# Performance work log

Measured on AMD Instinct MI355X. Metric: run time of the kernel, lower is better.

Reference implementation:

```python
import jax, jax.numpy as jnp
import numpy as np

D_MODEL = 1024
N_HEADS = 16
DIM_HEAD = D_MODEL // N_HEADS
SCALE = DIM_HEAD ** (-0.5)
B, T = 8, 1024


def setup_inputs() -> dict:
    key = jax.random.key(0)
    k1, k2, k3 = jax.random.split(key, 3)
    x = jax.random.normal(k1, (B, T, D_MODEL), dtype=jnp.float32)
    m = jnp.ones((B, T), dtype=jnp.float32)  # padding mask (1 = keep)
    w_qkv = jax.random.normal(k2, (3 * D_MODEL, D_MODEL), dtype=jnp.float32) * (D_MODEL ** -0.5)
    w_out = jax.random.normal(k3, (D_MODEL, D_MODEL), dtype=jnp.float32) * (D_MODEL ** -0.5)
    b_out = jnp.zeros((D_MODEL,), dtype=jnp.float32)
    return {"x": x, "m": m, "w_qkv": w_qkv, "w_out": w_out, "b_out": b_out, "l": T}


def reference(x, m, w_qkv, w_out, b_out, l):
    b, t, dm = x.shape
    qkv = jnp.einsum('btd,ed->bte', x, w_qkv)  # (b,t,3*d_model)
    q, k, v = jnp.split(qkv, 3, axis=-1)
    rs = lambda a: a.reshape(b, t, N_HEADS, DIM_HEAD)
    q, k, v = rs(q), rs(k), rs(v)
    e = jnp.einsum('bihd,bjhd->bijh', q, k) * SCALE  # (b,i,j,h)
    # combined padding + causal mask
    kpm = m[:, :, None] * m[:, None, :]              # (b,i,j)
    kpm = jnp.tril(kpm)[..., None]                   # (b,i,j,1)
    neg = -jnp.finfo(e.dtype).max
    e = jnp.where(kpm == 0, neg, e)
    a = jax.nn.softmax(e, axis=2)                    # softmax over j
    o = jnp.einsum('bijh,bjhd->bihd', a, v).reshape(b, t, dm)
    o = jnp.einsum('btd,ed->bte', o, w_out) + b_out
    # dropout is identity in eval mode
    return o * m[..., None]
```

## Files before the change

### kernel.cpp

```cpp
#include <hip/hip_runtime.h>
#include <cstdint>
#include <cstddef>

typedef unsigned short u16;
typedef __bf16 bf16;
typedef bf16 __attribute__((ext_vector_type(4))) bf16x4;
typedef bf16 __attribute__((ext_vector_type(8))) bf16x8;
typedef float __attribute__((ext_vector_type(4))) f32x4;
typedef u16 __attribute__((ext_vector_type(8))) u16x8;

#define QSCALE 0.18033688011112042f

__device__ __forceinline__ u16 f2b(float x) {
  unsigned u = __float_as_uint(x);
  unsigned r = (u + 0x7fffu + ((u >> 16) & 1u)) >> 16;
  return (u16)r;
}

__device__ __forceinline__ void gl_lds16(const void* g, void* lds) {
  __builtin_amdgcn_global_load_lds(
      (const __attribute__((address_space(1))) unsigned int*)g,
      (__attribute__((address_space(3))) unsigned int*)lds, 16, 0, 0);
}

__device__ __forceinline__ bf16x8 frag(const u16* base, int row, int kchunk) {
  const int c = kchunk ^ (row & 7);
  return *(const bf16x8*)(base + row * 64 + c * 8);
}
__device__ __forceinline__ void stage_tile4(const u16* gbase, int K, char* lbase,
                                            int wave, int lane) {
#pragma unroll
  for (int i = 0; i < 4; ++i) {
    const int q = wave * 64 + lane + i * 256;
    const int r = q >> 3, c = (q & 7) ^ (r & 7);
    gl_lds16(gbase + (size_t)r * K + c * 8, lbase + i * 4096 + wave * 1024);
  }
}

__device__ __forceinline__ bf16x8 frag32(const u16* base, int row, int kchunk) {
  const int c = kchunk ^ ((row >> 1) & 3);
  return *(const bf16x8*)(base + row * 32 + c * 8);
}
__device__ __forceinline__ void stage32(const u16* gbase, int K, char* lbase,
                                        int wave, int lane) {
  const int q0 = wave * 64 + lane;
  const int r0 = q0 >> 2, c0 = (q0 & 3) ^ ((r0 >> 1) & 3);
  gl_lds16(gbase + (size_t)r0 * K + c0 * 8, lbase + wave * 1024);
  const int q1 = q0 + 256;
  const int r1 = q1 >> 2, c1 = (q1 & 3) ^ ((r1 >> 1) & 3);
  gl_lds16(gbase + (size_t)r1 * K + c1 * 8, lbase + 4096 + wave * 1024);
}

__global__ __launch_bounds__(256) void castk(const float* __restrict__ in,
                                             u16* __restrict__ out, int n) {
  int i = (blockIdx.x * 256 + threadIdx.x) * 8;
  if (i >= n) return;
  float4 a = *(const float4*)(in + i);
  float4 b = *(const float4*)(in + i + 4);
  u16x8 v;
  v[0] = f2b(a.x); v[1] = f2b(a.y); v[2] = f2b(a.z); v[3] = f2b(a.w);
  v[4] = f2b(b.x); v[5] = f2b(b.y); v[6] = f2b(b.z); v[7] = f2b(b.w);
  *(u16x8*)(out + i) = v;
}

__global__ __launch_bounds__(256, 4) void gemm_qkv(
    const u16* __restrict__ A, const u16* __restrict__ B,
    u16* __restrict__ Qo, u16* __restrict__ Ko, u16* __restrict__ Vo) {
  __shared__ u16 As[2][128 * 32];
  __shared__ u16 Bs[2][128 * 32];
  const int tid = threadIdx.x;
  const int lane = tid & 63, wave = tid >> 6;
  const int fr = lane & 15, fg = lane >> 4;
  const int wr = wave >> 1, wc = wave & 1;
  const int bid = blockIdx.x;
  const int bm = bid & 63, bn = bid >> 6;
  const int K = 1024;
  const u16* Ab = A + (size_t)bm * 128 * K;
  const u16* Bb = B + (size_t)bn * 128 * K;

  f32x4 acc[4][4] = {};

  stage32(Ab, K, (char*)&As[0][0], wave, lane);
  stage32(Bb, K, (char*)&Bs[0][0], wave, lane);
  __syncthreads();

  int cur = 0;
#pragma unroll 1
  for (int t = 0; t < 32; ++t) {
    if (t < 31) {
      stage32(Ab + (size_t)(t + 1) * 32, K, (char*)&As[cur ^ 1][0], wave, lane);
      stage32(Bb + (size_t)(t + 1) * 32, K, (char*)&Bs[cur ^ 1][0], wave, lane);
    }
    bf16x8 af[4], bfv[4];
#pragma unroll
    for (int mi = 0; mi < 4; ++mi)
      af[mi] = frag32(&As[cur][0], wr * 64 + mi * 16 + fr, fg);
#pragma unroll
    for (int ni = 0; ni < 4; ++ni)
      bfv[ni] = frag32(&Bs[cur][0], wc * 64 + ni * 16 + fr, fg);
#pragma unroll
    for (int mi = 0; mi < 4; ++mi)
#pragma unroll
      for (int ni = 0; ni < 4; ++ni)
        acc[mi][ni] = __builtin_amdgcn_mfma_f32_16x16x32_bf16(
            af[mi], bfv[ni], acc[mi][ni], 0, 0, 0);
    __syncthreads();
    cur ^= 1;
  }

  const int gr0 = bm * 128 + wr * 64;
  const int gc0 = bn * 128 + wc * 64;
#pragma unroll
  for (int mi = 0; mi < 4; ++mi) {
    const int rb = gr0 + mi * 16 + fg * 4;
    const int b = rb >> 10, t = rb & 1023;
#pragma unroll
    for (int ni = 0; ni < 4; ++ni) {
      const int c = gc0 + ni * 16 + fr;
      const int region = c >> 10, cc = c & 1023;
      const int h = cc >> 6, d = cc & 63;
      const size_t bh = (size_t)(b * 16 + h);
      if (region == 0) {
#pragma unroll
        for (int g = 0; g < 4; ++g)
          Qo[(bh * 1024 + t + g) * 64 + d] = f2b(acc[mi][ni][g] * QSCALE);
      } else if (region == 1) {
#pragma unroll
        for (int g = 0; g < 4; ++g)
          Ko[(bh * 1024 + t + g) * 64 + d] = f2b(acc[mi][ni][g]);
      } else {
        ushort4 pv;
        pv.x = f2b(acc[mi][ni][0]);
        pv.y = f2b(acc[mi][ni][1]);
        pv.z = f2b(acc[mi][ni][2]);
        pv.w = f2b(acc[mi][ni][3]);
        *(ushort4*)(Vo + (bh * 64 + d) * 1024 + t) = pv;
      }
    }
  }
}

__global__ __launch_bounds__(256) void gemm_bt2(
    const u16* __restrict__ A, const u16* __restrict__ B,
    float* __restrict__ Co, const float* __restrict__ bias,
    const float* __restrict__ msk) {
  __shared__ u16 As[2][128 * 64];
  __shared__ u16 Bs[2][128 * 64];
  const int tid = threadIdx.x;
  const int lane = tid & 63, wave = tid >> 6;
  const int fr = lane & 15, fg = lane >> 4;
  const int wr = wave >> 1, wc = wave & 1;
  const int bid = blockIdx.x;
  const int bm = bid & 63, bn = bid >> 6;
  const int K = 1024, N = 1024;
  const u16* Ab = A + (size_t)bm * 128 * K;
  const u16* Bb = B + (size_t)bn * 128 * K;

  f32x4 acc[4][4] = {};

  stage_tile4(Ab, K, (char*)&As[0][0], wave, lane);
  stage_tile4(Bb, K, (char*)&Bs[0][0], wave, lane);
  __syncthreads();

  int cur = 0;
#pragma unroll 1
  for (int t = 0; t < 16; ++t) {
    if (t < 15) {
      stage_tile4(Ab + (size_t)(t + 1) * 64, K, (char*)&As[cur ^ 1][0], wave, lane);
      stage_tile4(Bb + (size_t)(t + 1) * 64, K, (char*)&Bs[cur ^ 1][0], wave, lane);
    }
    bf16x8 af[4][2], bfv[4][2];
#pragma unroll
    for (int mi = 0; mi < 4; ++mi)
#pragma unroll
      for (int kk = 0; kk < 2; ++kk)
        af[mi][kk] = frag(&As[cur][0], wr * 64 + mi * 16 + fr, kk * 4 + fg);
#pragma unroll
    for (int ni = 0; ni < 4; ++ni)
#pragma unroll
      for (int kk = 0; kk < 2; ++kk)
        bfv[ni][kk] = frag(&Bs[cur][0], wc * 64 + ni * 16 + fr, kk * 4 + fg);
#pragma unroll
    for (int mi = 0; mi < 4; ++mi)
#pragma unroll
      for (int ni = 0; ni < 4; ++ni)
#pragma unroll
        for (int kk = 0; kk < 2; ++kk)
          acc[mi][ni] = __builtin_amdgcn_mfma_f32_16x16x32_bf16(
              af[mi][kk], bfv[ni][kk], acc[mi][ni], 0, 0, 0);
    __syncthreads();
    cur ^= 1;
  }

  const int gr0 = bm * 128 + wr * 64;
  const int gc0 = bn * 128 + wc * 64;
#pragma unroll
  for (int mi = 0; mi < 4; ++mi) {
    const int rb = gr0 + mi * 16 + fg * 4;
#pragma unroll
    for (int ni = 0; ni < 4; ++ni) {
      const int c = gc0 + ni * 16 + fr;
      const float bo = bias[c];
#pragma unroll
      for (int g = 0; g < 4; ++g) {
        const int r = rb + g;
        Co[(size_t)r * N + c] = (acc[mi][ni][g] + bo) * msk[r];
      }
    }
  }
}

__global__ __launch_bounds__(256) void attnk(const u16* __restrict__ Qb,
                                             const u16* __restrict__ Kb,
                                             const u16* __restrict__ Vtb,
                                             const float* __restrict__ msk,
                                             u16* __restrict__ Ob) {
  __shared__ u16 Ks[2][64 * 64];
  __shared__ u16 Vs[2][64 * 64];
  __shared__ u16 Ps[4][32 * 72];
  const int tid = threadIdx.x;
  const int lane = tid & 63, wave = tid >> 6;
  const int fr = lane & 15, fg = lane >> 4;
  const int bid = blockIdx.x;
  __constant__ static const int tab[8] = {7, 6, 0, 1, 5, 4, 2, 3};
  const int qi = tab[bid >> 7];
  const int bh = bid & 127;
  const int b = bh >> 4, h = bh & 15;
  const int qw = qi * 128 + wave * 32;

  bf16x8 qf[2][2];
#pragma unroll
  for (int ct = 0; ct < 2; ++ct)
#pragma unroll
    for (int kc = 0; kc < 2; ++kc)
      qf[ct][kc] = *(const bf16x8*)(Qb + ((size_t)bh * 1024 + qw + ct * 16 + fr) * 64 +
                                    kc * 32 + fg * 8);

  f32x4 o[2][4] = {};
  float mrun[2], lrun[2];
  mrun[0] = mrun[1] = -3.0e38f;
  lrun[0] = lrun[1] = 0.f;

  const int cc0 = wave * 64 + lane;
  const int krow0 = cc0 >> 3, kcb0 = (cc0 & 7) ^ (krow0 & 7);
  const int cc1 = 256 + cc0;
  const int krow1 = cc1 >> 3, kcb1 = (cc1 & 7) ^ (krow1 & 7);

  const int nkb = qi * 2 + 2;

  gl_lds16(Kb + ((size_t)bh * 1024 + krow0) * 64 + kcb0 * 8, (char*)&Ks[0][0] + wave * 1024);
  gl_lds16(Vtb + ((size_t)bh * 64 + krow0) * 1024 + kcb0 * 8, (char*)&Vs[0][0] + wave * 1024);
  gl_lds16(Kb + ((size_t)bh * 1024 + krow1) * 64 + kcb1 * 8, (char*)&Ks[0][0] + 4096 + wave * 1024);
  gl_lds16(Vtb + ((size_t)bh * 64 + krow1) * 1024 + kcb1 * 8, (char*)&Vs[0][0] + 4096 + wave * 1024);

#pragma unroll 1
  for (int kb = 0; kb < nkb; ++kb) {
    __syncthreads();
    if (kb + 1 < nkb) {
      char* kd = (char*)&Ks[(kb + 1) & 1][0];
      char* vd = (char*)&Vs[(kb + 1) & 1][0];
      gl_lds16(Kb + ((size_t)bh * 1024 + (kb + 1) * 64 + krow0) * 64 + kcb0 * 8, kd + wave * 1024);
      gl_lds16(Vtb + ((size_t)bh * 64 + krow0) * 1024 + (kb + 1) * 64 + kcb0 * 8, vd + wave * 1024);
      gl_lds16(Kb + ((size_t)bh * 1024 + (kb + 1) * 64 + krow1) * 64 + kcb1 * 8, kd + 4096 + wave * 1024);
      gl_lds16(Vtb + ((size_t)bh * 64 + krow1) * 1024 + (kb + 1) * 64 + kcb1 * 8, vd + 4096 + wave * 1024);
    }
    if (kb * 64 > qw + 31) continue;
    const u16* Kc = &Ks[kb & 1][0];
    const u16* Vc = &Vs[kb & 1][0];

    f32x4 st[2][4];
    const f32x4 z = {0.f, 0.f, 0.f, 0.f};
#pragma unroll
    for (int nt = 0; nt < 4; ++nt) {
      const int krow = nt * 16 + fr;
      const int cb0r = (0 * 4 + fg) ^ (krow & 7);
      const int cb1r = (1 * 4 + fg) ^ (krow & 7);
      const bf16x8 kf0 = *(const bf16x8*)(Kc + krow * 64 + cb0r * 8);
      const bf16x8 kf1 = *(const bf16x8*)(Kc + krow * 64 + cb1r * 8);
#pragma unroll
      for (int ct = 0; ct < 2; ++ct) {
        st[ct][nt] = __builtin_amdgcn_mfma_f32_16x16x32_bf16(kf0, qf[ct][0], z, 0, 0, 0);
        st[ct][nt] = __builtin_amdgcn_mfma_f32_16x16x32_bf16(kf1, qf[ct][1], st[ct][nt], 0, 0, 0);
      }
    }

    float kbias[4][4];
#pragma unroll
    for (int nt = 0; nt < 4; ++nt) {
      const float4 km4 = *(const float4*)(msk + b * 1024 + kb * 64 + nt * 16 + fg * 4);
      kbias[nt][0] = (km4.x == 0.f) ? -3.0e38f : 0.f;
      kbias[nt][1] = (km4.y == 0.f) ? -3.0e38f : 0.f;
      kbias[nt][2] = (km4.z == 0.f) ? -3.0e38f : 0.f;
      kbias[nt][3] = (km4.w == 0.f) ? -3.0e38f : 0.f;
    }
#pragma unroll
    for (int ct = 0; ct < 2; ++ct)
#pragma unroll
      for (int nt = 0; nt < 4; ++nt)
#pragma unroll
        for (int g = 0; g < 4; ++g) st[ct][nt][g] += kbias[nt][g];

    const bool edge = (kb * 64 + 63 > qw);
    if (edge) {
#pragma unroll
      for (int ct = 0; ct < 2; ++ct) {
        const int q = qw + ct * 16 + fr;
#pragma unroll
        for (int nt = 0; nt < 4; ++nt)
#pragma unroll
          for (int g = 0; g < 4; ++g) {
            const int j = kb * 64 + nt * 16 + fg * 4 + g;
            if (j > q) st[ct][nt][g] = -3.0e38f;
          }
      }
    }

    float sc[2];
#pragma unroll
    for (int ct = 0; ct < 2; ++ct) {
      float mx = st[ct][0][0];
#pragma unroll
      for (int nt = 0; nt < 4; ++nt)
#pragma unroll
        for (int g = 0; g < 4; ++g) mx = fmaxf(mx, st[ct][nt][g]);
      mx = fmaxf(mx, __shfl_xor(mx, 16));
      mx = fmaxf(mx, __shfl_xor(mx, 32));
      const float nm = fmaxf(mrun[ct], mx);
      sc[ct] = exp2f(mrun[ct] - nm);
      mrun[ct] = nm;
      float rs = 0.f;
#pragma unroll
      for (int nt = 0; nt < 4; ++nt)
#pragma unroll
        for (int g = 0; g < 4; ++g) {
          const float p = exp2f(st[ct][nt][g] - nm);
          st[ct][nt][g] = p;
          rs += p;
        }
      rs += __shfl_xor(rs, 16);
      rs += __shfl_xor(rs, 32);
      lrun[ct] = lrun[ct] * sc[ct] + rs;
#pragma unroll
      for (int nt = 0; nt < 4; ++nt) {
        bf16x4 pk;
        pk[0] = (bf16)st[ct][nt][0];
        pk[1] = (bf16)st[ct][nt][1];
        pk[2] = (bf16)st[ct][nt][2];
        pk[3] = (bf16)st[ct][nt][3];
        *(bf16x4*)(&Ps[wave][(ct * 16 + fr) * 72 + nt * 16 + fg * 4]) = pk;
      }
    }

#pragma unroll
    for (int mt = 0; mt < 2; ++mt)
#pragma unroll
      for (int g = 0; g < 4; ++g) {
        const float scr = __shfl(sc[mt], fg * 4 + g);
#pragma unroll
        for (int dt = 0; dt < 4; ++dt) o[mt][dt][g] *= scr;
      }

#pragma unroll
    for (int jc = 0; jc < 2; ++jc) {
      bf16x8 pa[2];
#pragma unroll
      for (int mt = 0; mt < 2; ++mt)
        pa[mt] = *(const bf16x8*)(&Ps[wave][(mt * 16 + fr) * 72 + jc * 32 + fg * 8]);
#pragma unroll
      for (int dt = 0; dt < 4; ++dt) {
        const int vrow = dt * 16 + fr;
        const int cb = (jc * 4 + fg) ^ (vrow & 7);
        const bf16x8 vf = *(const bf16x8*)(Vc + vrow * 64 + cb * 8);
#pragma unroll
        for (int mt = 0; mt < 2; ++mt)
          o[mt][dt] = __builtin_amdgcn_mfma_f32_16x16x32_bf16(pa[mt], vf, o[mt][dt], 0, 0, 0);
      }
    }
  }

  float inv[2];
  inv[0] = 1.0f / lrun[0];
  inv[1] = 1.0f / lrun[1];
#pragma unroll
  for (int mt = 0; mt < 2; ++mt)
#pragma unroll
    for (int g = 0; g < 4; ++g) {
      const float invr = __shfl(inv[mt], fg * 4 + g);
      const int q = qw + mt * 16 + fg * 4 + g;
#pragma unroll
      for (int dt = 0; dt < 4; ++dt)
        Ob[((size_t)b * 1024 + q) * 1024 + h * 64 + dt * 16 + fr] =
            f2b(o[mt][dt][g] * invr);
    }
}

extern "C" void kernel_launch(void* const* d_in, const int* in_sizes, int n_in,
                              void* d_out, int out_size, void* d_ws, size_t ws_size,
                              hipStream_t stream) {
  (void)in_sizes; (void)n_in; (void)out_size; (void)ws_size;
  const float* x = (const float*)d_in[0];
  const float* m = (const float*)d_in[1];
  const float* w_qkv = (const float*)d_in[2];
  const float* w_out = (const float*)d_in[3];
  const float* b_out = (const float*)d_in[4];
  float* out = (float*)d_out;

  char* ws = (char*)d_ws;
  const size_t MB = 1u << 20;
  u16* Xb    = (u16*)(ws + 0);
  u16* Wqkvb = (u16*)(ws + 16 * MB);
  u16* Woutb = (u16*)(ws + 22 * MB);
  u16* Qb    = (u16*)(ws + 24 * MB);
  u16* Kb    = (u16*)(ws + 40 * MB);
  u16* Vtb   = (u16*)(ws + 56 * MB);
  u16* Ob    = Xb;

  castk<<<4096, 256, 0, stream>>>(x, Xb, 8 * 1024 * 1024);
  castk<<<1536, 256, 0, stream>>>(w_qkv, Wqkvb, 3072 * 1024);
  castk<<<512, 256, 0, stream>>>(w_out, Woutb, 1024 * 1024);

  gemm_qkv<<<1536, 256, 0, stream>>>(Xb, Wqkvb, Qb, Kb, Vtb);

  attnk<<<1024, 256, 0, stream>>>(Qb, Kb, Vtb, m, Ob);

  gemm_bt2<<<512, 256, 0, stream>>>(Ob, Woutb, out, b_out, m);
}
```

Measured before the change: 175.0 us.

## Move P to registers via shuffles, add lazy softmax rescale, multiply mask

The attention kernel no longer writes P through per-wave LDS. It packs P into bf16 pairs and rearranges them into the MFMA A-operand layout with cross-lane shuffles. It also skips the running-max update and accumulator rescale when the new block max is within a threshold of the running max for the whole wave, and applies the key padding mask by multiplication after exp instead of adding a large negative bias. The aim is to remove LDS traffic and rescale ALU work, at the cost of many shuffle instructions and some divergence-dependent branching.

```diff
diff --git a/kernel.cpp b/kernel.cpp
--- a/kernel.cpp
+++ b/kernel.cpp
@@ -4,6 +4,7 @@
 
 typedef unsigned short u16;
 typedef __bf16 bf16;
+typedef bf16 __attribute__((ext_vector_type(2))) bf16x2;
 typedef bf16 __attribute__((ext_vector_type(4))) bf16x4;
 typedef bf16 __attribute__((ext_vector_type(8))) bf16x8;
 typedef float __attribute__((ext_vector_type(4))) f32x4;
@@ -217,7 +218,6 @@
                                              u16* __restrict__ Ob) {
   __shared__ u16 Ks[2][64 * 64];
   __shared__ u16 Vs[2][64 * 64];
-  __shared__ u16 Ps[4][32 * 72];
   const int tid = threadIdx.x;
   const int lane = tid & 63, wave = tid >> 6;
   const int fr = lane & 15, fg = lane >> 4;
@@ -240,6 +240,9 @@
   float mrun[2], lrun[2];
   mrun[0] = mrun[1] = -3.0e38f;
   lrun[0] = lrun[1] = 0.f;
+
+  const int src0 = fr + ((fg & 1) << 5);
+  const int src1 = src0 + 16;
 
   const int cc0 = wave * 64 + lane;
   const int krow0 = cc0 >> 3, kcb0 = (cc0 & 7) ^ (krow0 & 7);
@@ -284,21 +287,12 @@
       }
     }
 
-    float kbias[4][4];
+    float kmv[4][4];
 #pragma unroll
     for (int nt = 0; nt < 4; ++nt) {
       const float4 km4 = *(const float4*)(msk + b * 1024 + kb * 64 + nt * 16 + fg * 4);
-      kbias[nt][0] = (km4.x == 0.f) ? -3.0e38f : 0.f;
-      kbias[nt][1] = (km4.y == 0.f) ? -3.0e38f : 0.f;
-      kbias[nt][2] = (km4.z == 0.f) ? -3.0e38f : 0.f;
-      kbias[nt][3] = (km4.w == 0.f) ? -3.0e38f : 0.f;
-    }
-#pragma unroll
-    for (int ct = 0; ct < 2; ++ct)
-#pragma unroll
-      for (int nt = 0; nt < 4; ++nt)
-#pragma unroll
-        for (int g = 0; g < 4; ++g) st[ct][nt][g] += kbias[nt][g];
+      kmv[nt][0] = km4.x; kmv[nt][1] = km4.y; kmv[nt][2] = km4.z; kmv[nt][3] = km4.w;
+    }
 
     const bool edge = (kb * 64 + 63 > qw);
     if (edge) {
@@ -316,6 +310,7 @@
     }
 
     float sc[2];
+    int doR[2];
 #pragma unroll
     for (int ct = 0; ct < 2; ++ct) {
       float mx = st[ct][0][0];
@@ -325,47 +320,71 @@
         for (int g = 0; g < 4; ++g) mx = fmaxf(mx, st[ct][nt][g]);
       mx = fmaxf(mx, __shfl_xor(mx, 16));
       mx = fmaxf(mx, __shfl_xor(mx, 32));
-      const float nm = fmaxf(mrun[ct], mx);
-      sc[ct] = exp2f(mrun[ct] - nm);
-      mrun[ct] = nm;
+      float nm;
+      if (__all(mx <= mrun[ct] + 8.f)) {
+        nm = mrun[ct]; sc[ct] = 1.f; doR[ct] = 0;
+      } else {
+        nm = fmaxf(mrun[ct], mx);
+        sc[ct] = exp2f(mrun[ct] - nm);
+        mrun[ct] = nm; doR[ct] = 1;
+      }
       float rs = 0.f;
 #pragma unroll
       for (int nt = 0; nt < 4; ++nt)
 #pragma unroll
         for (int g = 0; g < 4; ++g) {
-          const float p = exp2f(st[ct][nt][g] - nm);
+          const float p = exp2f(st[ct][nt][g] - nm) * kmv[nt][g];
           st[ct][nt][g] = p;
           rs += p;
         }
       rs += __shfl_xor(rs, 16);
       rs += __shfl_xor(rs, 32);
-      lrun[ct] = lrun[ct] * sc[ct] + rs;
-#pragma unroll
-      for (int nt = 0; nt < 4; ++nt) {
-        bf16x4 pk;
-        pk[0] = (bf16)st[ct][nt][0];
-        pk[1] = (bf16)st[ct][nt][1];
-        pk[2] = (bf16)st[ct][nt][2];
-        pk[3] = (bf16)st[ct][nt][3];
-        *(bf16x4*)(&Ps[wave][(ct * 16 + fr) * 72 + nt * 16 + fg * 4]) = pk;
-      }
-    }
-
+      lrun[ct] = doR[ct] ? (lrun[ct] * sc[ct] + rs) : (lrun[ct] + rs);
+    }
+
+    int pk[2][4][2];
+#pragma unroll
+    for (int ct = 0; ct < 2; ++ct)
+#pragma unroll
+      for (int nt = 0; nt < 4; ++nt)
+#pragma unroll
+        for (int hh = 0; hh < 2; ++hh) {
+          bf16x2 tp;
+          tp[0] = (bf16)st[ct][nt][2 * hh];
+          tp[1] = (bf16)st[ct][nt][2 * hh + 1];
+          pk[ct][nt][hh] = __builtin_bit_cast(int, tp);
+        }
+
+    bf16x8 pa[2][2];
 #pragma unroll
     for (int mt = 0; mt < 2; ++mt)
 #pragma unroll
-      for (int g = 0; g < 4; ++g) {
-        const float scr = __shfl(sc[mt], fg * 4 + g);
-#pragma unroll
-        for (int dt = 0; dt < 4; ++dt) o[mt][dt][g] *= scr;
-      }
-
-#pragma unroll
-    for (int jc = 0; jc < 2; ++jc) {
-      bf16x8 pa[2];
-#pragma unroll
-      for (int mt = 0; mt < 2; ++mt)
-        pa[mt] = *(const bf16x8*)(&Ps[wave][(mt * 16 + fr) * 72 + jc * 32 + fg * 8]);
+      for (int jc = 0; jc < 2; ++jc) {
+        int w[4];
+#pragma unroll
+        for (int e2 = 0; e2 < 4; ++e2) {
+          const int sl = (e2 & 2) ? src1 : src0;
+          const int lo = __shfl(pk[mt][jc * 2 + 0][e2 & 1], sl);
+          const int hi = __shfl(pk[mt][jc * 2 + 1][e2 & 1], sl);
+          w[e2] = (fg & 2) ? hi : lo;
+        }
+        int4 wi = {w[0], w[1], w[2], w[3]};
+        pa[mt][jc] = __builtin_bit_cast(bf16x8, wi);
+      }
+
+#pragma unroll
+    for (int mt = 0; mt < 2; ++mt)
+      if (doR[mt]) {
+#pragma unroll
+        for (int g = 0; g < 4; ++g) {
+          const float scr = __shfl(sc[mt], fg * 4 + g);
+#pragma unroll
+          for (int dt = 0; dt < 4; ++dt) o[mt][dt][g] *= scr;
+        }
+      }
+
+#pragma unroll
+    for (int jc = 0; jc < 2; ++jc)
 #pragma unroll
       for (int dt = 0; dt < 4; ++dt) {
         const int vrow = dt * 16 + fr;
@@ -373,9 +392,8 @@
         const bf16x8 vf = *(const bf16x8*)(Vc + vrow * 64 + cb * 8);
 #pragma unroll
         for (int mt = 0; mt < 2; ++mt)
-          o[mt][dt] = __builtin_amdgcn_mfma_f32_16x16x32_bf16(pa[mt], vf, o[mt][dt], 0, 0, 0);
-      }
-    }
+          o[mt][dt] = __builtin_amdgcn_mfma_f32_16x16x32_bf16(pa[mt][jc], vf, o[mt][dt], 0, 0, 0);
+      }
   }
 
   float inv[2];
```

Result: faster. 170.9 us (-2.3%).
